# Kernel tuning notes

Measured on AMD Instinct MI355X. Metric: run time of the kernel, lower is better.

The kernel has to match this reference:

```python
import jax, jax.numpy as jnp
import numpy as np

SEQ, B, IN, H, OUT, L = 256, 64, 512, 1024, 256, 2
DT = 0.05

def setup_inputs() -> dict:
    key = jax.random.key(0)
    ks = jax.random.split(key, 10)
    s = lambda fan_in: 1.0 / np.sqrt(fan_in)
    return {
        "x":    jax.random.normal(ks[0], (SEQ, B, IN), dtype=jnp.float32),
        "W_in": jax.random.uniform(ks[1], (H, IN), jnp.float32, -s(IN), s(IN)),
        "b_in": jax.random.uniform(ks[2], (H,), jnp.float32, -s(IN), s(IN)),
        "W_c":  jax.random.uniform(ks[3], (H, 2 * H), jnp.float32, -s(2 * H), s(2 * H)),
        "b_c":  jax.random.uniform(ks[4], (H,), jnp.float32, -s(2 * H), s(2 * H)),
        "taus": jnp.ones((L,), jnp.float32),
        "W_o1": jax.random.uniform(ks[5], (H // 2, H), jnp.float32, -s(H), s(H)),
        "b_o1": jax.random.uniform(ks[6], (H // 2,), jnp.float32, -s(H), s(H)),
        "W_o2": jax.random.uniform(ks[7], (OUT, H // 2), jnp.float32, -s(H // 2), s(H // 2)),
        "b_o2": jax.random.uniform(ks[8], (OUT,), jnp.float32, -s(H // 2), s(H // 2)),
    }

def reference(x, W_in, b_in, W_c, b_c, taus, W_o1, b_o1, W_o2, b_o2):
    # input projection for all timesteps at once: [S,B,IN] -> [S,B,H]
    xp = jnp.einsum('sbi,hi->sbh', x, W_in) + b_in
    num_layers = taus.shape[0]
    batch = x.shape[1]
    hidden0 = jnp.zeros((num_layers, batch, W_in.shape[0]), dtype=x.dtype)

    def step(hidden, xt):
        inp = xt  # [B,H]
        new_hidden = []
        for layer in range(num_layers):
            h = hidden[layer]
            # original code calls cell(input_t.detach(), h): stop gradient on input path
            comb = jnp.concatenate([jax.lax.stop_gradient(inp), h], axis=-1)  # [B,2H]
            dhdt = jnp.tanh(comb @ W_c.T + b_c)
            h_next = h + (DT / (taus[layer] + 0.001)) * dhdt
            new_hidden.append(h_next)
            inp = h_next
        hidden = jnp.stack(new_hidden)  # [L,B,H]
        out = jax.nn.relu(hidden[-1] @ W_o1.T + b_o1) @ W_o2.T + b_o2  # [B,OUT]
        return hidden, out

    hidden_final, outputs = jax.lax.scan(step, hidden0, xp)
    return outputs, hidden_final
```

## Files before the change

kernel.cpp:

```cpp
#include <hip/hip_runtime.h>
#include <hip/hip_bf16.h>
#include <stdint.h>

typedef unsigned short ushort_t;
typedef unsigned long long ull_t;
using bf16x8 = __attribute__((ext_vector_type(8))) short;
using f32x4  = __attribute__((ext_vector_type(4))) float;

#define SEQ    256
#define BATCH  64
#define INDIM  512
#define HDIM   1024
#define OUTDIM 256
#define MTOT   (SEQ*BATCH)
#define BH     (BATCH*HDIM)
#define WPAD   1032
#define RSTR   324

__device__ __forceinline__ ushort_t f2bf(float f) {
  uint32_t u = __builtin_bit_cast(uint32_t, f);
  u += 0x7fffu + ((u >> 16) & 1u);
  return (ushort_t)(u >> 16);
}
__device__ __forceinline__ float bf2f(ushort_t b) {
  uint32_t u = ((uint32_t)b) << 16;
  return __builtin_bit_cast(float, u);
}
__device__ __forceinline__ f32x4 mfma16(bf16x8 a, bf16x8 b, f32x4 c) {
  return __builtin_amdgcn_mfma_f32_16x16x32_bf16(a, b, c, 0, 0, 0);
}
__device__ __forceinline__ void gload16(const void* g, void* l) {
  __builtin_amdgcn_global_load_lds(
      (const __attribute__((address_space(1))) unsigned int*)g,
      (__attribute__((address_space(3))) unsigned int*)l, 16, 0, 0);
}
__device__ __forceinline__ float tanhfast(float z) {
  float e = __expf(2.0f * z);
  return 1.0f - 2.0f / (e + 1.0f);
}
__device__ __forceinline__ int load_sc0_int(const int* p) {
  int v;
  asm volatile("global_load_dword %0, %1, off sc0\n\ts_waitcnt vmcnt(0)"
               : "=&v"(v) : "v"(p) : "memory");
  return v;
}
__device__ __forceinline__ void store_sc0_int(int* p, int v) {
  asm volatile("global_store_dword %0, %1, off sc0" :: "v"(p), "v"(v) : "memory");
}

__global__ void k_convert(const float* __restrict__ src, ushort_t* __restrict__ dst, int n) {
  int i = blockIdx.x * blockDim.x + threadIdx.x;
  if (i < n) dst[i] = f2bf(src[i]);
}
__global__ void k_split(const float* __restrict__ src, ushort_t* __restrict__ hi,
                        ushort_t* __restrict__ lo, int n) {
  int i = blockIdx.x * blockDim.x + threadIdx.x;
  if (i < n) {
    float v = src[i];
    ushort_t h = f2bf(v);
    hi[i] = h;
    lo[i] = f2bf(v - bf2f(h));
  }
}
__global__ void k_split_wc(const float* __restrict__ Wc,
                           ushort_t* __restrict__ WiH, ushort_t* __restrict__ WiL,
                           ushort_t* __restrict__ WhH, ushort_t* __restrict__ WhL) {
  int i = blockIdx.x * blockDim.x + threadIdx.x;
  if (i < HDIM * HDIM) {
    int row = i >> 10, k = i & 1023;
    float vi = Wc[(size_t)row * (2 * HDIM) + k];
    float vh = Wc[(size_t)row * (2 * HDIM) + HDIM + k];
    ushort_t ih = f2bf(vi);
    WiH[i] = ih; WiL[i] = f2bf(vi - bf2f(ih));
    ushort_t hh = f2bf(vh);
    WhH[i] = hh; WhL[i] = f2bf(vh - bf2f(hh));
  }
}

template<int SPLITB, int RELU, int OUTBF>
__global__ __launch_bounds__(256) void gemm_nt(
    const ushort_t* __restrict__ A, const ushort_t* __restrict__ Bhi,
    const ushort_t* __restrict__ Blo, const float* __restrict__ bias,
    float* __restrict__ Cf, ushort_t* __restrict__ Cb,
    int M, int N, int K)
{
  __shared__ ushort_t As[128 * 32];
  __shared__ ushort_t Bh[128 * 32];
  __shared__ ushort_t Bl[128 * 32];
  const int tid = threadIdx.x;
  const int w = tid >> 6, l = tid & 63;
  const int m0 = blockIdx.x * 128, n0 = blockIdx.y * 128;
  const int wr = w >> 1, wc = w & 1;
  const int lr = l & 15, lk = l >> 4;

  f32x4 acc[4][4] = {};
  const int nK = K >> 5;
  const size_t rowB = (size_t)K * 2;

  for (int kk = 0; kk < nK; ++kk) {
    const size_t kbyte = (size_t)kk * 64;
#pragma unroll
    for (int j = 0; j < 2; ++j) {
      int c = (w * 2 + j) * 64 + l;
      int row = c >> 2;
      int kb = (c & 3) * 16;
      gload16((const char*)A + (size_t)(m0 + row) * rowB + kbyte + kb,
              (char*)As + (w * 2 + j) * 1024);
      gload16((const char*)Bhi + (size_t)(n0 + row) * rowB + kbyte + kb,
              (char*)Bh + (w * 2 + j) * 1024);
      if (SPLITB)
        gload16((const char*)Blo + (size_t)(n0 + row) * rowB + kbyte + kb,
                (char*)Bl + (w * 2 + j) * 1024);
    }
    __syncthreads();
    bf16x8 af[4], bhf[4], blf[4];
#pragma unroll
    for (int i = 0; i < 4; ++i) {
      af[i]  = *(const bf16x8*)&As[(wr * 64 + i * 16 + lr) * 32 + lk * 8];
      bhf[i] = *(const bf16x8*)&Bh[(wc * 64 + i * 16 + lr) * 32 + lk * 8];
      if (SPLITB)
        blf[i] = *(const bf16x8*)&Bl[(wc * 64 + i * 16 + lr) * 32 + lk * 8];
    }
#pragma unroll
    for (int i = 0; i < 4; ++i)
#pragma unroll
      for (int j2 = 0; j2 < 4; ++j2) {
        acc[i][j2] = mfma16(af[i], bhf[j2], acc[i][j2]);
        if (SPLITB) acc[i][j2] = mfma16(af[i], blf[j2], acc[i][j2]);
      }
    __syncthreads();
  }
#pragma unroll
  for (int j2 = 0; j2 < 4; ++j2) {
    int n = n0 + wc * 64 + j2 * 16 + lr;
    float bv = bias ? bias[n] : 0.0f;
#pragma unroll
    for (int i = 0; i < 4; ++i) {
#pragma unroll
      for (int r = 0; r < 4; ++r) {
        int m = m0 + wr * 64 + i * 16 + lk * 4 + r;
        float v = acc[i][j2][r] + bv;
        if (RELU) v = fmaxf(v, 0.0f);
        if (OUTBF) Cb[(size_t)m * N + n] = f2bf(v);
        else       Cf[(size_t)m * N + n] = v;
      }
    }
  }
}

#define RIDX(buf, tile, q) ((((buf)*4 + (tile))*8 + (q)) * RSTR)
__global__ __attribute__((amdgpu_waves_per_eu(2, 2))) __launch_bounds__(512)
void scan_kernel(
    const float* __restrict__ P0,
    const ushort_t* __restrict__ WiH, const ushort_t* __restrict__ WiL,
    const ushort_t* __restrict__ WhH, const ushort_t* __restrict__ WhL,
    const float* __restrict__ b_c, const float* __restrict__ taus,
    ushort_t* __restrict__ h0buf,
    ushort_t* __restrict__ H1buf,
    float* __restrict__ outHidden, int* __restrict__ sync)
{
  __shared__ float red[2 * 4 * 8 * RSTR];
  __shared__ ushort_t WhLds[32 * WPAD];
  __shared__ int meta[2];
  __shared__ int dcnt;

  const int tid = threadIdx.x;
  const int w = tid >> 6, l = tid & 63;
  const int lr = l & 15, lk = l >> 4;

  int* cnt        = sync;
  int* flags_l2   = sync + 256;
  int* flags_mall = sync + 256 + 2048;

  if (tid == 0) {
    int xcd;
    asm volatile("s_getreg_b32 %0, hwreg(HW_REG_XCC_ID)" : "=s"(xcd));
    int slot = 999;
    if (xcd < 4)
      slot = __hip_atomic_fetch_add(&cnt[xcd], 1, __ATOMIC_RELAXED,
                                    __HIP_MEMORY_SCOPE_AGENT);
    meta[0] = (xcd < 4) ? xcd : -1;
    meta[1] = slot;
    dcnt = 0;
  }
  __syncthreads();
  const int g = meta[0];
  const int c = meta[1];
  if (g < 0 || c >= 32) return;

  const int rowg = g * 16, colg = c * 32;
  const int kb = w * 128;

  {
    const ushort_t* wsrc = WhH + (size_t)colg * HDIM;
#pragma unroll
    for (int j = 0; j < 8; ++j) {
      int e = (j * 512 + tid) * 8;
      bf16x8 v = *(const bf16x8*)&wsrc[e];
      *(bf16x8*)&WhLds[(e >> 10) * WPAD + (e & 1023)] = v;
    }
  }
  bf16x8 wl[2][4], wi[2][4];
#pragma unroll
  for (int ct = 0; ct < 2; ++ct)
#pragma unroll
    for (int kk = 0; kk < 4; ++kk) {
      size_t off = (size_t)(colg + ct * 16 + lr) * HDIM + kb + kk * 32 + lk * 8;
      wl[ct][kk] = *(const bf16x8*)&WhL[off];
      wi[ct][kk] = *(const bf16x8*)&WiH[off];
    }
  __syncthreads();

  const int* fl2p = &flags_l2[(g * 32 + w * 4 + (l & 3)) * 16];
  int*       fmlp = &flags_mall[(g * 32 + w * 4 + (l & 3)) * 16];

  const int ep = (w < 4);
  const int ph = w >> 1, ect = w & 1;
  const int ec = lr, R0 = lk * 4;
  float hm[4] = {0, 0, 0, 0};
  float bcn = 0.f, alpha = 0.f;
  float p0r[4] = {0, 0, 0, 0};
  if (ep) {
    alpha = 0.05f / (taus[ph] + 0.001f);
    bcn = b_c[colg + ect * 16 + ec];
    if (ph == 0) {
#pragma unroll
      for (int j = 0; j < 4; ++j)
        p0r[j] = P0[((size_t)0 * BATCH + rowg + R0 + j) * HDIM + colg + ect * 16 + ec];
    }
  }

  for (int i = 0; i <= SEQ; ++i) {
#pragma unroll
    for (int ct = 0; ct < 2; ++ct)
#pragma unroll
      for (int kk = 0; kk < 4; ++kk)
        asm volatile("" : "+v"(wl[ct][kk]), "+v"(wi[ct][kk]));

    if (i >= 1) {
      const int target = i;
      for (int r = 0;; ++r) {
        int v = 0x7fffffff;
        if (l < 4)
          v = ((r & 7) == 7)
            ? __hip_atomic_load(fmlp, __ATOMIC_RELAXED, __HIP_MEMORY_SCOPE_AGENT)
            : load_sc0_int(fl2p);
        if (__all(v >= target)) break;
      }
    }

    bf16x8 f[4] = {}, hh[4] = {};
    f32x4 aA[2] = {}, aI[2] = {}, aH[2] = {};
    if (i >= 1) {
      const ushort_t* h0r = h0buf + (size_t)(i - 1) * BH;
#pragma unroll
      for (int kk = 0; kk < 4; ++kk)
        f[kk] = *(const bf16x8*)&h0r[(size_t)(rowg + lr) * HDIM + kb + kk * 32 + lk * 8];
      if (i >= 2) {
        const ushort_t* h1r = H1buf + (size_t)(i - 2) * BH;
#pragma unroll
        for (int kk = 0; kk < 4; ++kk)
          hh[kk] = *(const bf16x8*)&h1r[(size_t)(rowg + lr) * HDIM + kb + kk * 32 + lk * 8];
      }
#pragma unroll
      for (int ct = 0; ct < 2; ++ct)
#pragma unroll
        for (int kk = 0; kk < 4; ++kk) {
          bf16x8 wh = *(const bf16x8*)&WhLds[(ct * 16 + lr) * WPAD + kb + kk * 32 + lk * 8];
          aA[ct] = mfma16(f[kk], wh, aA[ct]);
          aA[ct] = mfma16(f[kk], wl[ct][kk], aA[ct]);
          aI[ct] = mfma16(f[kk], wi[ct][kk], aI[ct]);
          if (i >= 2) {
            aH[ct] = mfma16(hh[kk], wh, aH[ct]);
            aH[ct] = mfma16(hh[kk], wl[ct][kk], aH[ct]);
          }
        }
    }
    const int buf = i & 1;
    const int wbase = lr * 20 + lk * 4;
#pragma unroll
    for (int ct = 0; ct < 2; ++ct) {
      *(f32x4*)&red[RIDX(buf, ct, w) + wbase] = aA[ct];
      f32x4 pb = aI[ct] + aH[ct];
      *(f32x4*)&red[RIDX(buf, 2 + ct, w) + wbase] = pb;
    }
    __syncthreads();

    if (ep) {
      const bool act = (ph == 0 && i < SEQ) || (ph == 1 && i >= 1);
      if (act) {
        f32x4 s = {};
        const float* rb = &red[RIDX(buf, w, 0) + ec * 20 + R0];
#pragma unroll
        for (int q = 0; q < 8; ++q)
          s += *(const f32x4*)&rb[q * RSTR];
        if (ph == 0) {
          ushort_t* dst = &h0buf[(size_t)i * BH + (size_t)(rowg + R0) * HDIM +
                                 colg + ect * 16 + ec];
#pragma unroll
          for (int j = 0; j < 4; ++j) {
            hm[j] += alpha * tanhfast(p0r[j] + s[j]);
            dst[(size_t)j * HDIM] = f2bf(hm[j]);
          }
        } else {
          ushort_t* dst = &H1buf[(size_t)(i - 1) * BH + (size_t)(rowg + R0) * HDIM +
                                 colg + ect * 16 + ec];
#pragma unroll
          for (int j = 0; j < 4; ++j) {
            hm[j] += alpha * tanhfast(s[j] + bcn);
            dst[(size_t)j * HDIM] = f2bf(hm[j]);
          }
        }
      }
      asm volatile("s_waitcnt vmcnt(0)" ::: "memory");
      if (i < SEQ && l == 0) {
        int old = __hip_atomic_fetch_add(&dcnt, 1, __ATOMIC_ACQ_REL,
                                         __HIP_MEMORY_SCOPE_WORKGROUP);
        if (old == 4 * i + 3) {
          store_sc0_int(&flags_l2[(g * 32 + c) * 16], i + 1);
          __hip_atomic_store(&flags_mall[(g * 32 + c) * 16], i + 1,
                             __ATOMIC_RELAXED, __HIP_MEMORY_SCOPE_AGENT);
        }
      }
      if (ph == 0 && i + 1 < SEQ) {
#pragma unroll
        for (int j = 0; j < 4; ++j)
          p0r[j] = P0[((size_t)(i + 1) * BATCH + rowg + R0 + j) * HDIM +
                      colg + ect * 16 + ec];
      }
    }
  }

  if (ep) {
    float* dst = &outHidden[(size_t)ph * BH + (size_t)(rowg + R0) * HDIM +
                            colg + ect * 16 + ec];
#pragma unroll
    for (int j = 0; j < 4; ++j) dst[(size_t)j * HDIM] = hm[j];
  }
}

extern "C" void kernel_launch(void* const* d_in, const int* in_sizes, int n_in,
                              void* d_out, int out_size, void* d_ws, size_t ws_size,
                              hipStream_t stream) {
  const float* x    = (const float*)d_in[0];
  const float* W_in = (const float*)d_in[1];
  const float* b_in = (const float*)d_in[2];
  const float* W_c  = (const float*)d_in[3];
  const float* b_c  = (const float*)d_in[4];
  const float* taus = (const float*)d_in[5];
  const float* W_o1 = (const float*)d_in[6];
  const float* b_o1 = (const float*)d_in[7];
  const float* W_o2 = (const float*)d_in[8];
  const float* b_o2 = (const float*)d_in[9];
  float* out = (float*)d_out;

  char* ws = (char*)d_ws;
  size_t off = 0;
  auto alloc = [&](size_t bytes) -> char* {
    char* p = ws + off;
    off += (bytes + 255) & ~(size_t)255;
    return p;
  };
  ushort_t* x_bf  = (ushort_t*)alloc((size_t)MTOT * INDIM * 2);
  ushort_t* xp_b  = (ushort_t*)alloc((size_t)MTOT * HDIM * 2);
  float*    P0    = (float*)   alloc((size_t)MTOT * HDIM * 4);
  ushort_t* H1buf = (ushort_t*)alloc((size_t)MTOT * HDIM * 2);
  ushort_t* h0buf = (ushort_t*)alloc((size_t)SEQ * BH * 2);
  ushort_t* O1    = (ushort_t*)alloc((size_t)MTOT * (HDIM/2) * 2);
  ushort_t* WiH   = (ushort_t*)alloc((size_t)HDIM * HDIM * 2);
  ushort_t* WiL   = (ushort_t*)alloc((size_t)HDIM * HDIM * 2);
  ushort_t* WhH   = (ushort_t*)alloc((size_t)HDIM * HDIM * 2);
  ushort_t* WhL   = (ushort_t*)alloc((size_t)HDIM * HDIM * 2);
  ushort_t* WinH  = (ushort_t*)alloc((size_t)HDIM * INDIM * 2);
  ushort_t* WinL  = (ushort_t*)alloc((size_t)HDIM * INDIM * 2);
  ushort_t* Wo1b  = (ushort_t*)alloc((size_t)(HDIM/2) * HDIM * 2);
  ushort_t* Wo2b  = (ushort_t*)alloc((size_t)OUTDIM * (HDIM/2) * 2);
  int*      sync  = (int*)     alloc(32768);
  if (off > ws_size) return;

  hipMemsetAsync(sync, 0, 32768, stream);

  k_convert<<<(MTOT * INDIM + 255) / 256, 256, 0, stream>>>(x, x_bf, MTOT * INDIM);
  k_split<<<(HDIM * INDIM + 255) / 256, 256, 0, stream>>>(W_in, WinH, WinL, HDIM * INDIM);
  k_split_wc<<<(HDIM * HDIM + 255) / 256, 256, 0, stream>>>(W_c, WiH, WiL, WhH, WhL);
  k_convert<<<((HDIM/2) * HDIM + 255) / 256, 256, 0, stream>>>(W_o1, Wo1b, (HDIM/2) * HDIM);
  k_convert<<<(OUTDIM * (HDIM/2) + 255) / 256, 256, 0, stream>>>(W_o2, Wo2b, OUTDIM * (HDIM/2));

  gemm_nt<1, 0, 1><<<dim3(MTOT / 128, HDIM / 128), 256, 0, stream>>>(
      x_bf, WinH, WinL, b_in, nullptr, xp_b, MTOT, HDIM, INDIM);
  gemm_nt<1, 0, 0><<<dim3(MTOT / 128, HDIM / 128), 256, 0, stream>>>(
      xp_b, WiH, WiL, b_c, P0, nullptr, MTOT, HDIM, HDIM);

  scan_kernel<<<512, 512, 0, stream>>>(P0, WiH, WiL, WhH, WhL, b_c, taus,
                                       h0buf, H1buf,
                                       out + (size_t)SEQ * BATCH * OUTDIM, sync);

  gemm_nt<0, 1, 1><<<dim3(MTOT / 128, (HDIM/2) / 128), 256, 0, stream>>>(
      H1buf, Wo1b, nullptr, b_o1, nullptr, O1, MTOT, HDIM / 2, HDIM);
  gemm_nt<0, 0, 0><<<dim3(MTOT / 128, OUTDIM / 128), 256, 0, stream>>>(
      O1, Wo2b, nullptr, b_o2, out, nullptr, MTOT, OUTDIM, HDIM / 2);
}
```

Before: 1.275 ms.

## Split scan work by layer phase with per-layer flags and pairwise split-K reduction

Restructures the persistent scan kernel. Each wave pair now owns one layer phase and column tile, and each wave covers half of K. The shared 8-way LDS reduction and block-wide __syncthreads are replaced by a pairwise LDS handoff with volatile flags. Separate global ready-flags per layer (A for h0, B for h1) are published per 16-column tile, so layer-0 and layer-1 consumers wait only on the data they need instead of a whole-block counter. This aims to cut the serial per-step barrier and reduction cost, at the price of more spin-waiting, more register-held weights (16 fragments), a second LDS weight copy and a larger sync buffer.

```diff
diff --git a/kernel.cpp b/kernel.cpp
--- a/kernel.cpp
+++ b/kernel.cpp
@@ -15,7 +15,6 @@
 #define MTOT   (SEQ*BATCH)
 #define BH     (BATCH*HDIM)
 #define WPAD   1032
-#define RSTR   324
 
 __device__ __forceinline__ ushort_t f2bf(float f) {
   uint32_t u = __builtin_bit_cast(uint32_t, f);
@@ -148,7 +147,6 @@
   }
 }
 
-#define RIDX(buf, tile, q) ((((buf)*4 + (tile))*8 + (q)) * RSTR)
 __global__ __attribute__((amdgpu_waves_per_eu(2, 2))) __launch_bounds__(512)
 void scan_kernel(
     const float* __restrict__ P0,
@@ -159,18 +157,22 @@
     ushort_t* __restrict__ H1buf,
     float* __restrict__ outHidden, int* __restrict__ sync)
 {
-  __shared__ float red[2 * 4 * 8 * RSTR];
-  __shared__ ushort_t WhLds[32 * WPAD];
+  __shared__ ushort_t WhHs[32 * WPAD];
+  __shared__ ushort_t WhLs[32 * WPAD];
+  __shared__ float slotf[4 * 64 * 4];
+  __shared__ int seqw[4];
+  __shared__ int epw[4];
   __shared__ int meta[2];
-  __shared__ int dcnt;
 
   const int tid = threadIdx.x;
   const int w = tid >> 6, l = tid & 63;
   const int lr = l & 15, lk = l >> 4;
 
-  int* cnt        = sync;
-  int* flags_l2   = sync + 256;
-  int* flags_mall = sync + 256 + 2048;
+  int* cnt = sync;
+  int* A_l2   = sync + 256;
+  int* A_mall = sync + 256 + 4096;
+  int* B_l2   = sync + 256 + 8192;
+  int* B_mall = sync + 256 + 12288;
 
   if (tid == 0) {
     int xcd;
@@ -181,159 +183,171 @@
                                     __HIP_MEMORY_SCOPE_AGENT);
     meta[0] = (xcd < 4) ? xcd : -1;
     meta[1] = slot;
-    dcnt = 0;
-  }
+  }
+  if (tid < 4) { seqw[tid] = 0; epw[tid] = 0; }
   __syncthreads();
   const int g = meta[0];
   const int c = meta[1];
   if (g < 0 || c >= 32) return;
 
   const int rowg = g * 16, colg = c * 32;
-  const int kb = w * 128;
+  const int pair = w & 3;
+  const int ph = pair >> 1;
+  const int ect = pair & 1;
+  const int half = w >> 2;
+  const int tc = colg + ect * 16;
 
   {
-    const ushort_t* wsrc = WhH + (size_t)colg * HDIM;
+    const ushort_t* s1 = WhH + (size_t)colg * HDIM;
+    const ushort_t* s2 = WhL + (size_t)colg * HDIM;
 #pragma unroll
     for (int j = 0; j < 8; ++j) {
       int e = (j * 512 + tid) * 8;
-      bf16x8 v = *(const bf16x8*)&wsrc[e];
-      *(bf16x8*)&WhLds[(e >> 10) * WPAD + (e & 1023)] = v;
-    }
-  }
-  bf16x8 wl[2][4], wi[2][4];
-#pragma unroll
-  for (int ct = 0; ct < 2; ++ct)
-#pragma unroll
-    for (int kk = 0; kk < 4; ++kk) {
-      size_t off = (size_t)(colg + ct * 16 + lr) * HDIM + kb + kk * 32 + lk * 8;
-      wl[ct][kk] = *(const bf16x8*)&WhL[off];
-      wi[ct][kk] = *(const bf16x8*)&WiH[off];
-    }
+      *(bf16x8*)&WhHs[(e >> 10) * WPAD + (e & 1023)] = *(const bf16x8*)&s1[e];
+      *(bf16x8*)&WhLs[(e >> 10) * WPAD + (e & 1023)] = *(const bf16x8*)&s2[e];
+    }
+  }
+  bf16x8 wreg[16];
+  {
+    const ushort_t* ws = (ph == 0) ? WhL : WiH;
+#pragma unroll
+    for (int kk = 0; kk < 16; ++kk)
+      wreg[kk] = *(const bf16x8*)&ws[(size_t)(tc + lr) * HDIM + half * 512 + kk * 32 + lk * 8];
+  }
   __syncthreads();
 
-  const int* fl2p = &flags_l2[(g * 32 + w * 4 + (l & 3)) * 16];
-  int*       fmlp = &flags_mall[(g * 32 + w * 4 + (l & 3)) * 16];
-
-  const int ep = (w < 4);
-  const int ph = w >> 1, ect = w & 1;
-  const int ec = lr, R0 = lk * 4;
+  const int* Apl = &A_l2[(g * 64 + l) * 16];
+  int*       Apm = &A_mall[(g * 64 + l) * 16];
+  const int* Bpl = &B_l2[(g * 64 + l) * 16];
+  int*       Bpm = &B_mall[(g * 64 + l) * 16];
+  int* myl2 = (ph == 0) ? &A_l2[(g * 64 + c * 2 + ect) * 16] : &B_l2[(g * 64 + c * 2 + ect) * 16];
+  int* myml = (ph == 0) ? &A_mall[(g * 64 + c * 2 + ect) * 16] : &B_mall[(g * 64 + c * 2 + ect) * 16];
+
   float hm[4] = {0, 0, 0, 0};
-  float bcn = 0.f, alpha = 0.f;
   float p0r[4] = {0, 0, 0, 0};
-  if (ep) {
-    alpha = 0.05f / (taus[ph] + 0.001f);
-    bcn = b_c[colg + ect * 16 + ec];
-    if (ph == 0) {
-#pragma unroll
-      for (int j = 0; j < 4; ++j)
-        p0r[j] = P0[((size_t)0 * BATCH + rowg + R0 + j) * HDIM + colg + ect * 16 + ec];
-    }
-  }
+  const float alpha = 0.05f / (taus[ph] + 0.001f);
+  const float bcn = b_c[tc + lr];
+  if (half == 0 && ph == 0) {
+#pragma unroll
+    for (int j = 0; j < 4; ++j)
+      p0r[j] = P0[((size_t)0 * BATCH + rowg + lk * 4 + j) * HDIM + tc + lr];
+  }
+
+  const int ldsrow = (ect * 16 + lr) * WPAD + half * 512;
 
   for (int i = 0; i <= SEQ; ++i) {
 #pragma unroll
-    for (int ct = 0; ct < 2; ++ct)
-#pragma unroll
-      for (int kk = 0; kk < 4; ++kk)
-        asm volatile("" : "+v"(wl[ct][kk]), "+v"(wi[ct][kk]));
+    for (int kk = 0; kk < 16; ++kk)
+      asm volatile("" : "+v"(wreg[kk]));
 
     if (i >= 1) {
-      const int target = i;
-      for (int r = 0;; ++r) {
-        int v = 0x7fffffff;
-        if (l < 4)
-          v = ((r & 7) == 7)
-            ? __hip_atomic_load(fmlp, __ATOMIC_RELAXED, __HIP_MEMORY_SCOPE_AGENT)
-            : load_sc0_int(fl2p);
-        if (__all(v >= target)) break;
-      }
-    }
-
-    bf16x8 f[4] = {}, hh[4] = {};
-    f32x4 aA[2] = {}, aI[2] = {}, aH[2] = {};
+      if (half == 0) {
+        const int tA = i, tB = i - 1;
+        bool okA = false, okB = (ph == 0) || (i < 2);
+        int rr = 0;
+        do {
+          if (rr >= 2) __builtin_amdgcn_s_sleep(1);
+          if (!okA) {
+            int v = ((rr & 7) == 7)
+              ? __hip_atomic_load(Apm, __ATOMIC_RELAXED, __HIP_MEMORY_SCOPE_AGENT)
+              : load_sc0_int(Apl);
+            okA = (__all(v >= tA) != 0);
+          }
+          if (!okB) {
+            int v = ((rr & 7) == 7)
+              ? __hip_atomic_load(Bpm, __ATOMIC_RELAXED, __HIP_MEMORY_SCOPE_AGENT)
+              : load_sc0_int(Bpl);
+            okB = (__all(v >= tB) != 0);
+          }
+          ++rr;
+        } while (!(okA && okB));
+        *(volatile int*)&epw[pair] = i;
+      } else {
+        int ev;
+        do { ev = *(volatile int*)&epw[pair]; } while (ev < i);
+      }
+    }
+
+    f32x4 acc = {};
     if (i >= 1) {
-      const ushort_t* h0r = h0buf + (size_t)(i - 1) * BH;
-#pragma unroll
-      for (int kk = 0; kk < 4; ++kk)
-        f[kk] = *(const bf16x8*)&h0r[(size_t)(rowg + lr) * HDIM + kb + kk * 32 + lk * 8];
-      if (i >= 2) {
-        const ushort_t* h1r = H1buf + (size_t)(i - 2) * BH;
-#pragma unroll
-        for (int kk = 0; kk < 4; ++kk)
-          hh[kk] = *(const bf16x8*)&h1r[(size_t)(rowg + lr) * HDIM + kb + kk * 32 + lk * 8];
-      }
-#pragma unroll
-      for (int ct = 0; ct < 2; ++ct)
-#pragma unroll
-        for (int kk = 0; kk < 4; ++kk) {
-          bf16x8 wh = *(const bf16x8*)&WhLds[(ct * 16 + lr) * WPAD + kb + kk * 32 + lk * 8];
-          aA[ct] = mfma16(f[kk], wh, aA[ct]);
-          aA[ct] = mfma16(f[kk], wl[ct][kk], aA[ct]);
-          aI[ct] = mfma16(f[kk], wi[ct][kk], aI[ct]);
-          if (i >= 2) {
-            aH[ct] = mfma16(hh[kk], wh, aH[ct]);
-            aH[ct] = mfma16(hh[kk], wl[ct][kk], aH[ct]);
-          }
+      const ushort_t* h0p = h0buf + (size_t)(i - 1) * BH +
+                            (size_t)(rowg + lr) * HDIM + half * 512 + lk * 8;
+      if (ph == 0) {
+#pragma unroll
+        for (int kk = 0; kk < 16; ++kk) {
+          bf16x8 f  = *(const bf16x8*)&h0p[kk * 32];
+          bf16x8 wh = *(const bf16x8*)&WhHs[ldsrow + kk * 32 + lk * 8];
+          acc = mfma16(f, wh, acc);
+          acc = mfma16(f, wreg[kk], acc);
         }
-    }
-    const int buf = i & 1;
-    const int wbase = lr * 20 + lk * 4;
-#pragma unroll
-    for (int ct = 0; ct < 2; ++ct) {
-      *(f32x4*)&red[RIDX(buf, ct, w) + wbase] = aA[ct];
-      f32x4 pb = aI[ct] + aH[ct];
-      *(f32x4*)&red[RIDX(buf, 2 + ct, w) + wbase] = pb;
-    }
-    __syncthreads();
-
-    if (ep) {
-      const bool act = (ph == 0 && i < SEQ) || (ph == 1 && i >= 1);
-      if (act) {
-        f32x4 s = {};
-        const float* rb = &red[RIDX(buf, w, 0) + ec * 20 + R0];
-#pragma unroll
-        for (int q = 0; q < 8; ++q)
-          s += *(const f32x4*)&rb[q * RSTR];
-        if (ph == 0) {
-          ushort_t* dst = &h0buf[(size_t)i * BH + (size_t)(rowg + R0) * HDIM +
-                                 colg + ect * 16 + ec];
-#pragma unroll
-          for (int j = 0; j < 4; ++j) {
-            hm[j] += alpha * tanhfast(p0r[j] + s[j]);
-            dst[(size_t)j * HDIM] = f2bf(hm[j]);
-          }
-        } else {
-          ushort_t* dst = &H1buf[(size_t)(i - 1) * BH + (size_t)(rowg + R0) * HDIM +
-                                 colg + ect * 16 + ec];
-#pragma unroll
-          for (int j = 0; j < 4; ++j) {
-            hm[j] += alpha * tanhfast(s[j] + bcn);
-            dst[(size_t)j * HDIM] = f2bf(hm[j]);
-          }
+      } else if (i >= 2) {
+        const ushort_t* h1p = H1buf + (size_t)(i - 2) * BH +
+                              (size_t)(rowg + lr) * HDIM + half * 512 + lk * 8;
+#pragma unroll
+        for (int kk = 0; kk < 16; ++kk) {
+          bf16x8 f   = *(const bf16x8*)&h0p[kk * 32];
+          bf16x8 hh  = *(const bf16x8*)&h1p[kk * 32];
+          bf16x8 whh = *(const bf16x8*)&WhHs[ldsrow + kk * 32 + lk * 8];
+          bf16x8 whl = *(const bf16x8*)&WhLs[ldsrow + kk * 32 + lk * 8];
+          acc = mfma16(f, wreg[kk], acc);
+          acc = mfma16(hh, whh, acc);
+          acc = mfma16(hh, whl, acc);
         }
+      } else {
+#pragma unroll
+        for (int kk = 0; kk < 16; ++kk) {
+          bf16x8 f = *(const bf16x8*)&h0p[kk * 32];
+          acc = mfma16(f, wreg[kk], acc);
+        }
+      }
+    }
+
+    const bool active = (ph == 0) ? (i < SEQ) : (i >= 1);
+    const bool red_on = active && (i >= 1);
+
+    if (half == 1) {
+      if (red_on) {
+        *(f32x4*)&slotf[(pair * 64 + l) * 4] = acc;
+        asm volatile("s_waitcnt lgkmcnt(0)" ::: "memory");
+        if (l == 0) *(volatile int*)&seqw[pair] = i + 1;
+      }
+    } else if (active) {
+      if (red_on) {
+        int sv;
+        do { sv = *(volatile int*)&seqw[pair]; } while (sv <= i);
+        acc += *(const f32x4*)&slotf[(pair * 64 + l) * 4];
+      }
+      if (ph == 0) {
+        ushort_t* dst = &h0buf[(size_t)i * BH + (size_t)(rowg + lk * 4) * HDIM + tc + lr];
+#pragma unroll
+        for (int j = 0; j < 4; ++j) {
+          hm[j] += alpha * tanhfast(p0r[j] + acc[j]);
+          dst[(size_t)j * HDIM] = f2bf(hm[j]);
+        }
+      } else {
+        ushort_t* dst = &H1buf[(size_t)(i - 1) * BH + (size_t)(rowg + lk * 4) * HDIM + tc + lr];
+#pragma unroll
+        for (int j = 0; j < 4; ++j) {
+          hm[j] += alpha * tanhfast(acc[j] + bcn);
+          dst[(size_t)j * HDIM] = f2bf(hm[j]);
+        }
       }
       asm volatile("s_waitcnt vmcnt(0)" ::: "memory");
-      if (i < SEQ && l == 0) {
-        int old = __hip_atomic_fetch_add(&dcnt, 1, __ATOMIC_ACQ_REL,
-                                         __HIP_MEMORY_SCOPE_WORKGROUP);
-        if (old == 4 * i + 3) {
-          store_sc0_int(&flags_l2[(g * 32 + c) * 16], i + 1);
-          __hip_atomic_store(&flags_mall[(g * 32 + c) * 16], i + 1,
-                             __ATOMIC_RELAXED, __HIP_MEMORY_SCOPE_AGENT);
-        }
+      if (l == 0) {
+        const int fv = (ph == 0) ? (i + 1) : i;
+        store_sc0_int(myl2, fv);
+        __hip_atomic_store(myml, fv, __ATOMIC_RELAXED, __HIP_MEMORY_SCOPE_AGENT);
       }
       if (ph == 0 && i + 1 < SEQ) {
 #pragma unroll
         for (int j = 0; j < 4; ++j)
-          p0r[j] = P0[((size_t)(i + 1) * BATCH + rowg + R0 + j) * HDIM +
-                      colg + ect * 16 + ec];
-      }
-    }
-  }
-
-  if (ep) {
-    float* dst = &outHidden[(size_t)ph * BH + (size_t)(rowg + R0) * HDIM +
-                            colg + ect * 16 + ec];
+          p0r[j] = P0[((size_t)(i + 1) * BATCH + rowg + lk * 4 + j) * HDIM + tc + lr];
+      }
+    }
+  }
+
+  if (half == 0) {
+    float* dst = &outHidden[(size_t)ph * BH + (size_t)(rowg + lk * 4) * HDIM + tc + lr];
 #pragma unroll
     for (int j = 0; j < 4; ++j) dst[(size_t)j * HDIM] = hm[j];
   }
@@ -375,10 +389,10 @@
   ushort_t* WinL  = (ushort_t*)alloc((size_t)HDIM * INDIM * 2);
   ushort_t* Wo1b  = (ushort_t*)alloc((size_t)(HDIM/2) * HDIM * 2);
   ushort_t* Wo2b  = (ushort_t*)alloc((size_t)OUTDIM * (HDIM/2) * 2);
-  int*      sync  = (int*)     alloc(32768);
+  int*      sync  = (int*)     alloc(131072);
   if (off > ws_size) return;
 
-  hipMemsetAsync(sync, 0, 32768, stream);
+  hipMemsetAsync(sync, 0, 131072, stream);
 
   k_convert<<<(MTOT * INDIM + 255) / 256, 256, 0, stream>>>(x, x_bf, MTOT * INDIM);
   k_split<<<(HDIM * INDIM + 255) / 256, 256, 0, stream>>>(W_in, WinH, WinL, HDIM * INDIM);
```

Result: slower. 2.352 ms (+84.6%).
